# Kernel tuning notes

Hardware: AMD Instinct MI355X
Metric: run time of the kernel (lower is better)

## Reference

```python
import jax, jax.numpy as jnp
import numpy as np

N = 100000
E = 1600000
D_IN = 128
D_HID = 128


def setup_inputs() -> dict:
    key = jax.random.key(0)
    ks = jax.random.split(key, 10)
    x = jax.random.normal(ks[0], (N, D_IN), dtype=jnp.float32)
    edge_index = jax.random.randint(ks[1], (2, E), 0, N, dtype=jnp.int64)
    def lin(k, i, o):
        kw, kb = jax.random.split(k)
        s = 1.0 / np.sqrt(i)
        return (jax.random.uniform(kw, (o, i), jnp.float32, -s, s),
                jax.random.uniform(kb, (o,), jnp.float32, -s, s))
    w0a, b0a = lin(ks[2], D_IN, D_HID)
    w0b, b0b = lin(ks[3], D_HID, D_HID)
    w1a, b1a = lin(ks[4], D_HID, D_HID)
    w1b, b1b = lin(ks[5], D_HID, D_HID)
    return {"x": x, "edge_index": edge_index,
            "w0a": w0a, "b0a": b0a, "w0b": w0b, "b0b": b0b,
            "w1a": w1a, "b1a": b1a, "w1b": w1b, "b1b": b1b}


def _gin_layer(x, src, dst, wa, ba, wb, bb):
    # GINConv, eps=0: h_i = x_i + sum_{j in N(i)} x_j (messages from src aggregated at dst)
    agg = jax.ops.segment_sum(x[src], dst, num_segments=N)  # [N, D]
    h = x + agg
    h = jax.nn.relu(h @ wa.T + ba)  # LinearBlock (no bn, no dropout)
    return h @ wb.T + bb            # final Linear of local_nn


def reference(x, edge_index, w0a, b0a, w0b, b0b, w1a, b1a, w1b, b1b):
    src, dst = edge_index[0], edge_index[1]
    h = _gin_layer(x, src, dst, w0a, b0a, w0b, b0b)
    h = _gin_layer(h, src, dst, w1a, b1a, w1b, b1b)
    return h
```

## Files before the change

kernel.cpp:

```cpp
#include <hip/hip_runtime.h>


typedef __attribute__((ext_vector_type(8))) short bf16x8;
typedef __attribute__((ext_vector_type(4))) float floatx4;

#define WS_ALIGN(x) (((x) + 255) & ~(size_t)255)
#define NBMAX 400
#define BCAP 6144

__device__ __forceinline__ unsigned short f2b(float f) {
  unsigned u = __builtin_bit_cast(unsigned, f);
  u = (u + 0x7FFF + ((u >> 16) & 1)) >> 16;
  return (unsigned short)u;
}
__device__ __forceinline__ float b2f(unsigned u16) {
  return __builtin_bit_cast(float, u16 << 16);
}

__global__ __launch_bounds__(256) void bucket_split(const int* __restrict__ src,
                                                    const int* __restrict__ dst,
                                                    int* __restrict__ bcnt,
                                                    unsigned* __restrict__ barr, int E, int nb) {
  __shared__ int cnt[NBMAX], base[NBMAX], cur[NBMAX];
  int t = threadIdx.x;
  for (int i = t; i < nb; i += 256) { cnt[i] = 0; cur[i] = 0; }
  __syncthreads();
  int e0 = blockIdx.x * 8192;
  int s[32], d[32];
#pragma unroll
  for (int k = 0; k < 32; k++) {
    int e = e0 + k * 256 + t;
    if (e < E) { s[k] = src[e]; d[k] = dst[e]; } else { d[k] = -1; }
  }
#pragma unroll
  for (int k = 0; k < 32; k++)
    if (d[k] >= 0) atomicAdd(&cnt[d[k] >> 8], 1);
  __syncthreads();
  for (int i = t; i < nb; i += 256) base[i] = cnt[i] ? atomicAdd(&bcnt[i], cnt[i]) : 0;
  __syncthreads();
#pragma unroll
  for (int k = 0; k < 32; k++)
    if (d[k] >= 0) {
      int b = d[k] >> 8;
      int r = atomicAdd(&cur[b], 1);
      barr[(size_t)b * BCAP + base[b] + r] = ((unsigned)(d[k] & 255) << 17) | (unsigned)s[k];
    }
}

__global__ void bucket_scan(const int* __restrict__ bcnt, int* __restrict__ sbase, int nb,
                            int* __restrict__ rowptr, int n) {
  __shared__ int buf[512];
  int t = threadIdx.x;
  int v = (t < nb) ? bcnt[t] : 0;
  buf[t] = v;
  __syncthreads();
  for (int off = 1; off < 512; off <<= 1) {
    int add = (t >= off) ? buf[t - off] : 0;
    __syncthreads();
    buf[t] += add;
    __syncthreads();
  }
  if (t < nb) sbase[t] = buf[t] - v;
  if (t == nb - 1) { sbase[nb] = buf[t]; rowptr[n] = buf[t]; }
}

__global__ __launch_bounds__(256) void bucket_csr(const unsigned* __restrict__ barr,
                                                  const int* __restrict__ bcnt,
                                                  const int* __restrict__ sbase,
                                                  int* __restrict__ rowptr, int* __restrict__ srt,
                                                  int n) {
  __shared__ int cnt[256], off[256], off2[256];
  int b = blockIdx.x, t = threadIdx.x;
  int cb = bcnt[b];
  int node0 = b * 256;
  int nlocal = min(256, n - node0);
  cnt[t] = 0;
  off2[t] = 0;
  __syncthreads();
  const unsigned* bp = barr + (size_t)b * BCAP;
  for (int i = t; i < cb; i += 256) atomicAdd(&cnt[bp[i] >> 17], 1);
  __syncthreads();
  int v = cnt[t];
  off[t] = v;
  __syncthreads();
  for (int o = 1; o < 256; o <<= 1) {
    int add = (t >= o) ? off[t - o] : 0;
    __syncthreads();
    off[t] += add;
    __syncthreads();
  }
  int excl = off[t] - v;
  int sb = sbase[b];
  if (t < nlocal) rowptr[node0 + t] = sb + excl;
  cnt[t] = excl;
  __syncthreads();
  for (int i = t; i < cb; i += 256) {
    unsigned pk = bp[i];
    int local = pk >> 17;
    int r = atomicAdd(&off2[local], 1);
    srt[sb + cnt[local] + r] = pk & 0x1FFFF;
  }
}

__global__ void cvt_kernel(const float* __restrict__ x, unsigned short* __restrict__ xb, int n4) {
  int i = blockIdx.x * blockDim.x + threadIdx.x;
  if (i < n4) {
    float4 v = ((const float4*)x)[i];
    uint2 pk;
    pk.x = (unsigned)f2b(v.x) | ((unsigned)f2b(v.y) << 16);
    pk.y = (unsigned)f2b(v.z) | ((unsigned)f2b(v.w) << 16);
    ((uint2*)xb)[i] = pk;
  }
}

__global__ __launch_bounds__(256) void aggregate_bf16(const unsigned short* __restrict__ X,
                                                      const int* __restrict__ rowptr,
                                                      const int* __restrict__ srt,
                                                      unsigned short* __restrict__ out, int n) {
  int w = blockIdx.x * 4 + (threadIdx.x >> 6);
  if (w >= n) return;
  int lane = threadIdx.x & 63;
  int c = lane & 15;
  int s = lane >> 4;
  const uint4* Xv = (const uint4*)X;

  float acc[8];
#pragma unroll
  for (int i = 0; i < 8; i++) acc[i] = 0.f;

  if (s == 0) {
    uint4 u = Xv[(size_t)w * 16 + c];
    acc[0] += b2f(u.x & 0xffff); acc[1] += b2f(u.x >> 16);
    acc[2] += b2f(u.y & 0xffff); acc[3] += b2f(u.y >> 16);
    acc[4] += b2f(u.z & 0xffff); acc[5] += b2f(u.z >> 16);
    acc[6] += b2f(u.w & 0xffff); acc[7] += b2f(u.w >> 16);
  }

  int p0 = rowptr[w], e = rowptr[w + 1];
  int trips = (e - p0 + 3) >> 2;
  int idx = p0 + s;
#pragma unroll 2
  for (int i = 0; i < trips; i++, idx += 4) {
    bool valid = idx < e;
    int r = srt[valid ? idx : (e - 1)];
    uint4 u = Xv[(size_t)r * 16 + c];
    if (!valid) { u.x = 0; u.y = 0; u.z = 0; u.w = 0; }
    acc[0] += b2f(u.x & 0xffff); acc[1] += b2f(u.x >> 16);
    acc[2] += b2f(u.y & 0xffff); acc[3] += b2f(u.y >> 16);
    acc[4] += b2f(u.z & 0xffff); acc[5] += b2f(u.z >> 16);
    acc[6] += b2f(u.w & 0xffff); acc[7] += b2f(u.w >> 16);
  }

#pragma unroll
  for (int i = 0; i < 8; i++) {
    acc[i] += __shfl_xor(acc[i], 16, 64);
    acc[i] += __shfl_xor(acc[i], 32, 64);
  }

  unsigned pk = (unsigned)f2b(acc[2 * s]) | ((unsigned)f2b(acc[2 * s + 1]) << 16);
  ((unsigned*)out)[(size_t)w * 64 + c * 4 + s] = pk;
}

__device__ __forceinline__ void stage_w(char* buf, const float* __restrict__ W, int t) {
  for (int idx = t; idx < 2048; idx += 512) {
    int nrow = idx >> 4, c = idx & 15;
    float4 a = ((const float4*)W)[idx * 2];
    float4 b = ((const float4*)W)[idx * 2 + 1];
    uint4 pk;
    pk.x = (unsigned)f2b(a.x) | ((unsigned)f2b(a.y) << 16);
    pk.y = (unsigned)f2b(a.z) | ((unsigned)f2b(a.w) << 16);
    pk.z = (unsigned)f2b(b.x) | ((unsigned)f2b(b.y) << 16);
    pk.w = (unsigned)f2b(b.z) | ((unsigned)f2b(b.w) << 16);
    *(uint4*)(buf + nrow * 256 + ((c ^ (nrow & 15)) << 4)) = pk;
  }
}

template <int OUT_BF16>
__global__ __launch_bounds__(512) void mlp_kernel(
    const unsigned short* __restrict__ A, const float* __restrict__ Wa,
    const float* __restrict__ ba, const float* __restrict__ Wb,
    const float* __restrict__ bb, void* __restrict__ Cout, int n) {
  __shared__ __align__(16) char lds[65536];
  char* bufA = lds;
  char* bufB = lds + 32768;
  int t = threadIdx.x;
  stage_w(bufA, Wa, t);
  stage_w(bufB, Wb, t);

  int wave = t >> 6, lane = t & 63;
  int m = lane & 15, q = lane >> 4;
  int rbase = blockIdx.x * 128;
  int rowA = rbase + wave * 16 + m;
  int rA = rowA < n ? rowA : (n - 1);

  bf16x8 af[4];
  const bf16x8* Arow = (const bf16x8*)(A + (size_t)rA * 128);
#pragma unroll
  for (int ks = 0; ks < 4; ks++) af[ks] = Arow[ks * 4 + q];

  __syncthreads();

  floatx4 acc[8];
  floatx4 zf = {0.f, 0.f, 0.f, 0.f};
#pragma unroll
  for (int j = 0; j < 8; j++) acc[j] = zf;
#pragma unroll
  for (int ks = 0; ks < 4; ks++) {
#pragma unroll
    for (int j = 0; j < 8; j++) {
      bf16x8 bf = *(const bf16x8*)(bufA + (j * 16 + m) * 256 + (((ks * 4 + q) ^ m) << 4));
      acc[j] = __builtin_amdgcn_mfma_f32_16x16x32_bf16(af[ks], bf, acc[j], 0, 0, 0);
    }
  }
  __syncthreads();

#pragma unroll
  for (int j = 0; j < 8; j++) {
    float bias = ba[j * 16 + m];
#pragma unroll
    for (int reg = 0; reg < 4; reg++) {
      float v = fmaxf(acc[j][reg] + bias, 0.f);
      int lr = wave * 16 + q * 4 + reg;
      int col = j * 16 + m;
      *(unsigned short*)(bufA + lr * 256 + (((col >> 3) ^ (lr & 15)) << 4) + (col & 7) * 2) =
          f2b(v);
    }
  }
  __syncthreads();

  int lrA = wave * 16 + m;
#pragma unroll
  for (int ks = 0; ks < 4; ks++)
    af[ks] = *(const bf16x8*)(bufA + lrA * 256 + (((ks * 4 + q) ^ m) << 4));
#pragma unroll
  for (int j = 0; j < 8; j++) acc[j] = zf;
#pragma unroll
  for (int ks = 0; ks < 4; ks++) {
#pragma unroll
    for (int j = 0; j < 8; j++) {
      bf16x8 bf = *(const bf16x8*)(bufB + (j * 16 + m) * 256 + (((ks * 4 + q) ^ m) << 4));
      acc[j] = __builtin_amdgcn_mfma_f32_16x16x32_bf16(af[ks], bf, acc[j], 0, 0, 0);
    }
  }

#pragma unroll
  for (int j = 0; j < 8; j++) {
    float bias = bb[j * 16 + m];
#pragma unroll
    for (int reg = 0; reg < 4; reg++) {
      int row = rbase + wave * 16 + q * 4 + reg;
      if (row >= n) continue;
      float v = acc[j][reg] + bias;
      int col = j * 16 + m;
      if (OUT_BF16)
        ((unsigned short*)Cout)[(size_t)row * 128 + col] = f2b(v);
      else
        ((float*)Cout)[(size_t)row * 128 + col] = v;
    }
  }
}

extern "C" void kernel_launch(void* const* d_in, const int* in_sizes, int n_in,
                              void* d_out, int out_size, void* d_ws, size_t ws_size,
                              hipStream_t stream) {
  const float* x   = (const float*)d_in[0];
  const int*   ei  = (const int*)d_in[1];
  const float* w0a = (const float*)d_in[2];
  const float* b0a = (const float*)d_in[3];
  const float* w0b = (const float*)d_in[4];
  const float* b0b = (const float*)d_in[5];
  const float* w1a = (const float*)d_in[6];
  const float* b1a = (const float*)d_in[7];
  const float* w1b = (const float*)d_in[8];
  const float* b1b = (const float*)d_in[9];
  float* out = (float*)d_out;

  int n = in_sizes[0] / 128;
  int E = in_sizes[1] / 2;
  const int* src = ei;
  const int* dst = ei + E;
  int nb = (n + 255) / 256;

  char* w = (char*)d_ws;
  int* rowptr = (int*)w;           w += WS_ALIGN((size_t)(n + 1) * 4);
  int* sbase = (int*)w;            w += WS_ALIGN((size_t)(NBMAX + 1) * 4);
  int* bcnt = (int*)w;             w += WS_ALIGN((size_t)NBMAX * 4);
  int* srt = (int*)w;              w += WS_ALIGN((size_t)E * 4);
  unsigned short* xb = (unsigned short*)w;  w += WS_ALIGN((size_t)n * 128 * 2);
  unsigned* barr = (unsigned*)w;
  unsigned short* B1 = (unsigned short*)w;

  hipMemsetAsync(bcnt, 0, (size_t)nb * 4, stream);
  bucket_split<<<(E + 8191) / 8192, 256, 0, stream>>>(src, dst, bcnt, barr, E, nb);
  bucket_scan<<<1, 512, 0, stream>>>(bcnt, sbase, nb, rowptr, n);
  bucket_csr<<<nb, 256, 0, stream>>>(barr, bcnt, sbase, rowptr, srt, n);

  cvt_kernel<<<(n * 32 + 255) / 256, 256, 0, stream>>>(x, xb, n * 32);

  int agg_grid = (n + 3) / 4;
  int mlp_grid = (n + 127) / 128;

  aggregate_bf16<<<agg_grid, 256, 0, stream>>>(xb, rowptr, srt, B1, n);
  mlp_kernel<1><<<mlp_grid, 512, 0, stream>>>(B1, w0a, b0a, w0b, b0b, xb, n);

  aggregate_bf16<<<agg_grid, 256, 0, stream>>>(xb, rowptr, srt, B1, n);
  mlp_kernel<0><<<mlp_grid, 512, 0, stream>>>(B1, w1a, b1a, w1b, b1b, out, n);
}
```

Baseline: 333.5 us.

## Fuse neighbor aggregation into MLP kernel and precompute swizzled bf16 weight images

Merges the separate gather-aggregate kernel into the per-layer MLP kernel, so aggregated rows are written directly into LDS instead of round-tripping through a global bf16 buffer. Weights are converted to swizzled bf16 once by a small kernel and copied straight into LDS, and a single weight buffer is reused for both linear layers to halve weight LDS. Each wave now aggregates 16 nodes sequentially rather than one node per wave, which cuts parallelism and latency hiding in the gather phase. The launch bound now requests more resident blocks per CU.

```diff
diff --git a/kernel.cpp b/kernel.cpp
--- a/kernel.cpp
+++ b/kernel.cpp
@@ -113,92 +113,97 @@
   }
 }
 
-__global__ __launch_bounds__(256) void aggregate_bf16(const unsigned short* __restrict__ X,
-                                                      const int* __restrict__ rowptr,
-                                                      const int* __restrict__ srt,
-                                                      unsigned short* __restrict__ out, int n) {
-  int w = blockIdx.x * 4 + (threadIdx.x >> 6);
-  if (w >= n) return;
-  int lane = threadIdx.x & 63;
-  int c = lane & 15;
-  int s = lane >> 4;
-  const uint4* Xv = (const uint4*)X;
-
-  float acc[8];
-#pragma unroll
-  for (int i = 0; i < 8; i++) acc[i] = 0.f;
-
-  if (s == 0) {
-    uint4 u = Xv[(size_t)w * 16 + c];
-    acc[0] += b2f(u.x & 0xffff); acc[1] += b2f(u.x >> 16);
-    acc[2] += b2f(u.y & 0xffff); acc[3] += b2f(u.y >> 16);
-    acc[4] += b2f(u.z & 0xffff); acc[5] += b2f(u.z >> 16);
-    acc[6] += b2f(u.w & 0xffff); acc[7] += b2f(u.w >> 16);
-  }
-
-  int p0 = rowptr[w], e = rowptr[w + 1];
-  int trips = (e - p0 + 3) >> 2;
-  int idx = p0 + s;
-#pragma unroll 2
-  for (int i = 0; i < trips; i++, idx += 4) {
-    bool valid = idx < e;
-    int r = srt[valid ? idx : (e - 1)];
-    uint4 u = Xv[(size_t)r * 16 + c];
-    if (!valid) { u.x = 0; u.y = 0; u.z = 0; u.w = 0; }
-    acc[0] += b2f(u.x & 0xffff); acc[1] += b2f(u.x >> 16);
-    acc[2] += b2f(u.y & 0xffff); acc[3] += b2f(u.y >> 16);
-    acc[4] += b2f(u.z & 0xffff); acc[5] += b2f(u.z >> 16);
-    acc[6] += b2f(u.w & 0xffff); acc[7] += b2f(u.w >> 16);
-  }
-
-#pragma unroll
-  for (int i = 0; i < 8; i++) {
-    acc[i] += __shfl_xor(acc[i], 16, 64);
-    acc[i] += __shfl_xor(acc[i], 32, 64);
-  }
-
-  unsigned pk = (unsigned)f2b(acc[2 * s]) | ((unsigned)f2b(acc[2 * s + 1]) << 16);
-  ((unsigned*)out)[(size_t)w * 64 + c * 4 + s] = pk;
-}
-
-__device__ __forceinline__ void stage_w(char* buf, const float* __restrict__ W, int t) {
-  for (int idx = t; idx < 2048; idx += 512) {
-    int nrow = idx >> 4, c = idx & 15;
-    float4 a = ((const float4*)W)[idx * 2];
-    float4 b = ((const float4*)W)[idx * 2 + 1];
-    uint4 pk;
-    pk.x = (unsigned)f2b(a.x) | ((unsigned)f2b(a.y) << 16);
-    pk.y = (unsigned)f2b(a.z) | ((unsigned)f2b(a.w) << 16);
-    pk.z = (unsigned)f2b(b.x) | ((unsigned)f2b(b.y) << 16);
-    pk.w = (unsigned)f2b(b.z) | ((unsigned)f2b(b.w) << 16);
-    *(uint4*)(buf + nrow * 256 + ((c ^ (nrow & 15)) << 4)) = pk;
-  }
+__global__ void wcvt_kernel(const float* __restrict__ w0, const float* __restrict__ w1,
+                            const float* __restrict__ w2, const float* __restrict__ w3,
+                            uint4* __restrict__ img) {
+  const float* W = (blockIdx.y == 0) ? w0 : (blockIdx.y == 1) ? w1 : (blockIdx.y == 2) ? w2 : w3;
+  int idx = blockIdx.x * 256 + threadIdx.x;
+  int nrow = idx >> 4, c = idx & 15;
+  float4 a = ((const float4*)W)[idx * 2];
+  float4 b = ((const float4*)W)[idx * 2 + 1];
+  uint4 pk;
+  pk.x = (unsigned)f2b(a.x) | ((unsigned)f2b(a.y) << 16);
+  pk.y = (unsigned)f2b(a.z) | ((unsigned)f2b(a.w) << 16);
+  pk.z = (unsigned)f2b(b.x) | ((unsigned)f2b(b.y) << 16);
+  pk.w = (unsigned)f2b(b.z) | ((unsigned)f2b(b.w) << 16);
+  img[(size_t)blockIdx.y * 2048 + nrow * 16 + (c ^ (nrow & 15))] = pk;
 }
 
 template <int OUT_BF16>
-__global__ __launch_bounds__(512) void mlp_kernel(
-    const unsigned short* __restrict__ A, const float* __restrict__ Wa,
-    const float* __restrict__ ba, const float* __restrict__ Wb,
+__global__ __launch_bounds__(512, 4) void layer_kernel(
+    const unsigned short* __restrict__ X, const int* __restrict__ rowptr,
+    const int* __restrict__ srt, const uint4* __restrict__ WaImg,
+    const float* __restrict__ ba, const uint4* __restrict__ WbImg,
     const float* __restrict__ bb, void* __restrict__ Cout, int n) {
   __shared__ __align__(16) char lds[65536];
   char* bufA = lds;
-  char* bufB = lds + 32768;
+  char* bufW = lds + 32768;
   int t = threadIdx.x;
-  stage_w(bufA, Wa, t);
-  stage_w(bufB, Wb, t);
-
   int wave = t >> 6, lane = t & 63;
+
+#pragma unroll
+  for (int r = 0; r < 4; r++) ((uint4*)bufW)[t + r * 512] = WaImg[t + r * 512];
+
+  {
+    int c = lane & 15, s = lane >> 4;
+    int coff = c * 16;
+    const char* Xb = (const char*)X;
+    int node0 = blockIdx.x * 128 + wave * 16;
+    for (int i = 0; i < 16; i++) {
+      int node = node0 + i;
+      if (node >= n) break;
+      float acc[8];
+#pragma unroll
+      for (int j = 0; j < 8; j++) acc[j] = 0.f;
+      if (s == 0) {
+        uint4 u = *(const uint4*)(Xb + (unsigned)node * 256 + coff);
+        acc[0] += b2f(u.x & 0xffff); acc[1] += b2f(u.x >> 16);
+        acc[2] += b2f(u.y & 0xffff); acc[3] += b2f(u.y >> 16);
+        acc[4] += b2f(u.z & 0xffff); acc[5] += b2f(u.z >> 16);
+        acc[6] += b2f(u.w & 0xffff); acc[7] += b2f(u.w >> 16);
+      }
+      int p0 = rowptr[node], e = rowptr[node + 1];
+      int cnt = e - p0;
+      int trips = cnt >> 2;
+      int idx = p0 + s;
+#pragma unroll 2
+      for (int it = 0; it < trips; it++, idx += 4) {
+        int r = srt[idx];
+        uint4 u = *(const uint4*)(Xb + (unsigned)r * 256 + coff);
+        acc[0] += b2f(u.x & 0xffff); acc[1] += b2f(u.x >> 16);
+        acc[2] += b2f(u.y & 0xffff); acc[3] += b2f(u.y >> 16);
+        acc[4] += b2f(u.z & 0xffff); acc[5] += b2f(u.z >> 16);
+        acc[6] += b2f(u.w & 0xffff); acc[7] += b2f(u.w >> 16);
+      }
+      int rem = cnt & 3;
+      if (s < rem) {
+        int r = srt[p0 + trips * 4 + s];
+        uint4 u = *(const uint4*)(Xb + (unsigned)r * 256 + coff);
+        acc[0] += b2f(u.x & 0xffff); acc[1] += b2f(u.x >> 16);
+        acc[2] += b2f(u.y & 0xffff); acc[3] += b2f(u.y >> 16);
+        acc[4] += b2f(u.z & 0xffff); acc[5] += b2f(u.z >> 16);
+        acc[6] += b2f(u.w & 0xffff); acc[7] += b2f(u.w >> 16);
+      }
+#pragma unroll
+      for (int j = 0; j < 8; j++) {
+        acc[j] += __shfl_xor(acc[j], 16, 64);
+        acc[j] += __shfl_xor(acc[j], 32, 64);
+      }
+      int lr = wave * 16 + i;
+      unsigned pk = (unsigned)f2b(acc[2 * s]) | ((unsigned)f2b(acc[2 * s + 1]) << 16);
+      *(unsigned*)(bufA + lr * 256 + ((c ^ (lr & 15)) << 4) + s * 4) = pk;
+    }
+  }
+  __syncthreads();
+
   int m = lane & 15, q = lane >> 4;
   int rbase = blockIdx.x * 128;
-  int rowA = rbase + wave * 16 + m;
-  int rA = rowA < n ? rowA : (n - 1);
+  int lrA = wave * 16 + m;
 
   bf16x8 af[4];
-  const bf16x8* Arow = (const bf16x8*)(A + (size_t)rA * 128);
-#pragma unroll
-  for (int ks = 0; ks < 4; ks++) af[ks] = Arow[ks * 4 + q];
-
-  __syncthreads();
+#pragma unroll
+  for (int ks = 0; ks < 4; ks++)
+    af[ks] = *(const bf16x8*)(bufA + lrA * 256 + (((ks * 4 + q) ^ m) << 4));
 
   floatx4 acc[8];
   floatx4 zf = {0.f, 0.f, 0.f, 0.f};
@@ -208,7 +213,7 @@
   for (int ks = 0; ks < 4; ks++) {
 #pragma unroll
     for (int j = 0; j < 8; j++) {
-      bf16x8 bf = *(const bf16x8*)(bufA + (j * 16 + m) * 256 + (((ks * 4 + q) ^ m) << 4));
+      bf16x8 bf = *(const bf16x8*)(bufW + (j * 16 + m) * 256 + (((ks * 4 + q) ^ m) << 4));
       acc[j] = __builtin_amdgcn_mfma_f32_16x16x32_bf16(af[ks], bf, acc[j], 0, 0, 0);
     }
   }
@@ -226,9 +231,10 @@
           f2b(v);
     }
   }
-  __syncthreads();
-
-  int lrA = wave * 16 + m;
+#pragma unroll
+  for (int r = 0; r < 4; r++) ((uint4*)bufW)[t + r * 512] = WbImg[t + r * 512];
+  __syncthreads();
+
 #pragma unroll
   for (int ks = 0; ks < 4; ks++)
     af[ks] = *(const bf16x8*)(bufA + lrA * 256 + (((ks * 4 + q) ^ m) << 4));
@@ -238,7 +244,7 @@
   for (int ks = 0; ks < 4; ks++) {
 #pragma unroll
     for (int j = 0; j < 8; j++) {
-      bf16x8 bf = *(const bf16x8*)(bufB + (j * 16 + m) * 256 + (((ks * 4 + q) ^ m) << 4));
+      bf16x8 bf = *(const bf16x8*)(bufW + (j * 16 + m) * 256 + (((ks * 4 + q) ^ m) << 4));
       acc[j] = __builtin_amdgcn_mfma_f32_16x16x32_bf16(af[ks], bf, acc[j], 0, 0, 0);
     }
   }
@@ -287,8 +293,11 @@
   int* bcnt = (int*)w;             w += WS_ALIGN((size_t)NBMAX * 4);
   int* srt = (int*)w;              w += WS_ALIGN((size_t)E * 4);
   unsigned short* xb = (unsigned short*)w;  w += WS_ALIGN((size_t)n * 128 * 2);
+  uint4* wimg = (uint4*)w;         w += WS_ALIGN((size_t)4 * 32768);
   unsigned* barr = (unsigned*)w;
-  unsigned short* B1 = (unsigned short*)w;
+  unsigned short* y1 = (unsigned short*)w;
+
+  wcvt_kernel<<<dim3(8, 4), 256, 0, stream>>>(w0a, w0b, w1a, w1b, wimg);
 
   hipMemsetAsync(bcnt, 0, (size_t)nb * 4, stream);
   bucket_split<<<(E + 8191) / 8192, 256, 0, stream>>>(src, dst, bcnt, barr, E, nb);
@@ -297,12 +306,8 @@
 
   cvt_kernel<<<(n * 32 + 255) / 256, 256, 0, stream>>>(x, xb, n * 32);
 
-  int agg_grid = (n + 3) / 4;
-  int mlp_grid = (n + 127) / 128;
-
-  aggregate_bf16<<<agg_grid, 256, 0, stream>>>(xb, rowptr, srt, B1, n);
-  mlp_kernel<1><<<mlp_grid, 512, 0, stream>>>(B1, w0a, b0a, w0b, b0b, xb, n);
-
-  aggregate_bf16<<<agg_grid, 256, 0, stream>>>(xb, rowptr, srt, B1, n);
-  mlp_kernel<0><<<mlp_grid, 512, 0, stream>>>(B1, w1a, b1a, w1b, b1b, out, n);
-}
+  int grid = (n + 127) / 128;
+  layer_kernel<1><<<grid, 512, 0, stream>>>(xb, rowptr, srt, wimg, b0a, wimg + 2048, b0b, y1, n);
+  layer_kernel<0><<<grid, 512, 0, stream>>>(y1, rowptr, srt, wimg + 4096, b1a, wimg + 6144, b1b,
+                                            out, n);
+}
```

New measurement: 400.6 us. 20.1% more time.
